# Optimization experiments

Measured on AMD Instinct MI355X. Metric: run time of the kernel, lower is better.

Reference implementation:

```python
import jax, jax.numpy as jnp
import numpy as np

N_NODES = 50000
N_EDGES = 800000
IN_FEATS = 128
H_FEATS = 128
OUT_FEATS = 64


def _mean_agg(h, src, dst, n_nodes):
    # mean over in-neighbors: sum h[src] into dst, divide by in-degree (0 for isolated nodes)
    summed = jax.ops.segment_sum(h[src], dst, num_segments=n_nodes)  # [N, d]
    deg = jax.ops.segment_sum(jnp.ones((src.shape[0],), h.dtype), dst, num_segments=n_nodes)
    return summed / jnp.maximum(deg, 1.0)[:, None]


def setup_inputs() -> dict:
    key = jax.random.key(0)
    ks = jax.random.split(key, 10)
    s = 0.05
    return {
        "inputs": jax.random.normal(ks[0], (N_NODES, IN_FEATS), jnp.float32),
        "fc_W": jax.random.normal(ks[1], (H_FEATS, IN_FEATS), jnp.float32) * s,
        "fc_b": jax.random.normal(ks[2], (H_FEATS,), jnp.float32) * s,
        "W": jax.random.normal(ks[3], (3, H_FEATS, H_FEATS), jnp.float32) * s,
        "b": jax.random.normal(ks[4], (3, H_FEATS), jnp.float32) * s,
        "W_last": jax.random.normal(ks[5], (OUT_FEATS, H_FEATS), jnp.float32) * s,
        "b_last": jax.random.normal(ks[6], (OUT_FEATS,), jnp.float32) * s,
        "eps": jnp.zeros((4,), jnp.float32),
        "src": jax.random.randint(ks[7], (N_EDGES,), 0, N_NODES, jnp.int32),
        "dst": jax.random.randint(ks[8], (N_EDGES,), 0, N_NODES, jnp.int32),
    }


def reference(inputs, fc_W, fc_b, W, b, W_last, b_last, eps, src, dst):
    n = inputs.shape[0]
    # input SLP
    h = jax.nn.relu(inputs @ fc_W.T + fc_b)
    # 3 hidden GIN layers: relu(Linear((1+eps)*h + mean_agg(h)))  (dropout = eval identity)
    for i in range(3):
        agg = _mean_agg(h, src, dst, n)
        h = jax.nn.relu(((1.0 + eps[i]) * h + agg) @ W[i].T + b[i])
    # last GIN layer (no ReLU)
    agg = _mean_agg(h, src, dst, n)
    h = ((1.0 + eps[3]) * h + agg) @ W_last.T + b_last
    return h
```

## Files before the change

### kernel.cpp

```cpp
#include <hip/hip_runtime.h>

#define N_NODES 50000
#define N_EDGES 800000
#define NBUCK 196
#define CAP 4608
#define CSTRIDE 16
#define EPB 2048
#define NSTRIPE ((N_EDGES + EPB - 1) / EPB)

typedef __attribute__((ext_vector_type(8))) short short8;
typedef __attribute__((ext_vector_type(4))) float float4v;

__device__ inline unsigned short f2bf(float f) {
    unsigned u = __float_as_uint(f);
    unsigned r = u + 0x7fff + ((u >> 16) & 1);
    return (unsigned short)(r >> 16);
}
__device__ inline float bf2f(unsigned short h) {
    return __uint_as_float(((unsigned)h) << 16);
}


__global__ void __launch_bounds__(256) wsplit_init(
    const float* __restrict__ fcW, const float* __restrict__ W, const float* __restrict__ Wl,
    unsigned short* __restrict__ hi, unsigned short* __restrict__ lo) {
    int i = blockIdx.x * 256 + threadIdx.x;
    float v;
    if (i < 16384) v = fcW[i];
    else if (i < 65536) v = W[i - 16384];
    else if (i < 73728) v = Wl[i - 65536];
    else return;
    unsigned short h = f2bf(v);
    hi[i] = h;
    lo[i] = f2bf(v - bf2f(h));
}


template <int COLS, bool RELU, bool WRITE_BF, bool BIAS, bool ASPLIT>
__device__ __forceinline__ void gemm_body(int bx, const float* __restrict__ U,
                                          const unsigned short* __restrict__ Uhi,
                                          const unsigned short* __restrict__ Ulo,
                                          const unsigned short* __restrict__ Whi,
                                          const unsigned short* __restrict__ Wlo,
                                          const float* __restrict__ bias, float* __restrict__ out,
                                          unsigned short* __restrict__ outbf, int nrows) {
    int wave = threadIdx.x >> 6;
    int lane = threadIdx.x & 63;
    int m = lane & 15;
    int quad = lane >> 4;
    int r0 = bx * 64 + wave * 16;
    int rowA = r0 + m;
    if (rowA >= nrows) rowA = nrows - 1;

    short8 ahi[4], alo[4];
    if (ASPLIT) {
        const unsigned short* hp = Uhi + (size_t)rowA * 128 + quad * 8;
        const unsigned short* lp = Ulo + (size_t)rowA * 128 + quad * 8;
#pragma unroll
        for (int kc = 0; kc < 4; kc++) {
            ahi[kc] = *(const short8*)(hp + kc * 32);
            alo[kc] = *(const short8*)(lp + kc * 32);
        }
    } else {
        const float* arow = U + (size_t)rowA * 128 + quad * 8;
#pragma unroll
        for (int kc = 0; kc < 4; kc++) {
            float4 f0 = *(const float4*)(arow + kc * 32);
            float4 f1 = *(const float4*)(arow + kc * 32 + 4);
            float fv[8] = {f0.x, f0.y, f0.z, f0.w, f1.x, f1.y, f1.z, f1.w};
#pragma unroll
            for (int j = 0; j < 8; j++) {
                unsigned short h = f2bf(fv[j]);
                ahi[kc][j] = (short)h;
                alo[kc][j] = (short)f2bf(fv[j] - bf2f(h));
            }
        }
    }

#pragma unroll
    for (int nt = 0; nt < COLS / 16; nt++) {
        int n = nt * 16 + m;
        const unsigned short* bhp = Whi + (size_t)n * 128 + quad * 8;
        const unsigned short* blp = Wlo + (size_t)n * 128 + quad * 8;
        float4v acc = {0.f, 0.f, 0.f, 0.f};
#pragma unroll
        for (int kc = 0; kc < 4; kc++) {
            short8 bh = *(const short8*)(bhp + kc * 32);
            short8 bl = *(const short8*)(blp + kc * 32);
            acc = __builtin_amdgcn_mfma_f32_16x16x32_bf16(ahi[kc], bh, acc, 0, 0, 0);
            acc = __builtin_amdgcn_mfma_f32_16x16x32_bf16(alo[kc], bh, acc, 0, 0, 0);
            acc = __builtin_amdgcn_mfma_f32_16x16x32_bf16(ahi[kc], bl, acc, 0, 0, 0);
        }
        float bv = 0.f;
        if (BIAS) bv = bias[n];
#pragma unroll
        for (int i = 0; i < 4; i++) {
            int r = r0 + quad * 4 + i;
            if (r < nrows) {
                float v = acc[i] + bv;
                if (RELU) v = fmaxf(v, 0.f);
                out[(size_t)r * COLS + n] = v;
                if (WRITE_BF) outbf[(size_t)r * COLS + n] = f2bf(v);
            }
        }
    }
}

template <int COLS, bool RELU, bool WRITE_BF, bool BIAS, bool ASPLIT>
__global__ void __launch_bounds__(256) gemm_mfma(const float* __restrict__ U,
                                                 const unsigned short* __restrict__ Uhi,
                                                 const unsigned short* __restrict__ Ulo,
                                                 const unsigned short* __restrict__ Whi,
                                                 const unsigned short* __restrict__ Wlo,
                                                 const float* __restrict__ bias,
                                                 float* __restrict__ out,
                                                 unsigned short* __restrict__ outbf, int nrows) {
    gemm_body<COLS, RELU, WRITE_BF, BIAS, ASPLIT>(blockIdx.x, U, Uhi, Ulo, Whi, Wlo, bias, out,
                                                  outbf, nrows);
}


__global__ void __launch_bounds__(256) fused_binA_gemm(
    const int* __restrict__ src, const int* __restrict__ dst, int* __restrict__ cursor,
    int* __restrict__ packed, const float* __restrict__ X, const unsigned short* __restrict__ whi,
    const unsigned short* __restrict__ wlo, const float* __restrict__ fcb, float* __restrict__ h,
    unsigned short* __restrict__ hbf) {
    int bx = blockIdx.x;
    if (bx < NSTRIPE) {
        __shared__ int lcount[256];
        __shared__ int lbase[256];
        int t = threadIdx.x;
        lcount[t] = 0;
        __syncthreads();
        int base = bx * EPB + t;
        int d[EPB / 256];
#pragma unroll
        for (int k = 0; k < EPB / 256; k++) {
            int i = base + k * 256;
            d[k] = (i < N_EDGES) ? dst[i] : -1;
            if (d[k] >= 0) atomicAdd(&lcount[((unsigned)d[k]) >> 8], 1);
        }
        __syncthreads();
        if (t < NBUCK) {
            lbase[t] = t * CAP + atomicAdd(&cursor[t * CSTRIDE], lcount[t]);
            lcount[t] = 0;
        }
        __syncthreads();
#pragma unroll
        for (int k = 0; k < EPB / 256; k++) {
            if (d[k] >= 0) {
                int i = base + k * 256;
                int wb = ((unsigned)d[k]) >> 8;
                int p = lbase[wb] + atomicAdd(&lcount[wb], 1);
                if (p < (wb + 1) * CAP)
                    packed[p] = ((d[k] & 255) << 16) | src[i];
            }
        }
    } else {
        gemm_body<128, true, true, true, false>(bx - NSTRIPE, X, nullptr, nullptr, whi, wlo, fcb,
                                                h, hbf, N_NODES);
    }
}


__global__ void __launch_bounds__(256) binB_kernel(const int* __restrict__ packed,
                                                   const int* __restrict__ cursor,
                                                   int* __restrict__ row_ptr,
                                                   int* __restrict__ esrc) {
    __shared__ int sm[256];
    __shared__ int cntS[256];
    __shared__ int curs[256];
    int b = blockIdx.x;
    int t = threadIdx.x;
    int cnt = (t < NBUCK) ? cursor[t * CSTRIDE] : 0;
    cntS[t] = cnt;
    sm[t] = cnt;
    __syncthreads();
    for (int o = 1; o < 256; o <<= 1) {
        int x = sm[t];
        int a = (t >= o) ? sm[t - o] : 0;
        __syncthreads();
        sm[t] = x + a;
        __syncthreads();
    }
    int w0 = sm[b] - cntS[b];
    int mycnt = cntS[b];
    int total = sm[NBUCK - 1];
    __syncthreads();
    if (b == NBUCK - 1 && t == 0) row_ptr[N_NODES] = total;
    int e0r = b * CAP, e1r = b * CAP + mycnt;
    curs[t] = 0;
    __syncthreads();
    for (int i = e0r + t; i < e1r; i += 256) atomicAdd(&curs[((unsigned)packed[i]) >> 16], 1);
    __syncthreads();
    int v = curs[t];
    sm[t] = v;
    __syncthreads();
    for (int o = 1; o < 256; o <<= 1) {
        int x = sm[t];
        int a = (t >= o) ? sm[t - o] : 0;
        __syncthreads();
        sm[t] = x + a;
        __syncthreads();
    }
    int excl = sm[t] - v;
    curs[t] = excl;
    int node = b * 256 + t;
    if (node < N_NODES) row_ptr[node] = w0 + excl;
    __syncthreads();
    for (int i = e0r + t; i < e1r; i += 256) {
        unsigned w = (unsigned)packed[i];
        int p = atomicAdd(&curs[w >> 16], 1);
        esrc[w0 + p] = (int)(w & 0xFFFFu);
    }
}


__global__ void __launch_bounds__(256) agg_kernel(
    const float* __restrict__ h, const unsigned short* __restrict__ hbf,
    const int* __restrict__ row_ptr, const int* __restrict__ esrc,
    const float* __restrict__ eps, int layer, unsigned* __restrict__ uhi32,
    unsigned* __restrict__ ulo32) {
    int gtid = blockIdx.x * 256 + threadIdx.x;
    int node = gtid >> 6;
    int lane = threadIdx.x & 63;
    if (node >= N_NODES) return;
    node = __builtin_amdgcn_readfirstlane(node);
    int beg = __builtin_amdgcn_readfirstlane(row_ptr[node]);
    int end = __builtin_amdgcn_readfirstlane(row_ptr[node + 1]);
    int eg = lane >> 4;
    int fo = lane & 15;

    float acc[8] = {0.f, 0.f, 0.f, 0.f, 0.f, 0.f, 0.f, 0.f};
    float acc2[8] = {0.f, 0.f, 0.f, 0.f, 0.f, 0.f, 0.f, 0.f};
    int e = beg;
    for (; e + 7 < end; e += 8) {
        int s0 = esrc[e + eg];
        int s1 = esrc[e + 4 + eg];
        short8 v0 = *(const short8*)(hbf + (size_t)s0 * 128 + fo * 8);
        short8 v1 = *(const short8*)(hbf + (size_t)s1 * 128 + fo * 8);
#pragma unroll
        for (int j = 0; j < 8; j++) acc[j] += bf2f((unsigned short)v0[j]);
#pragma unroll
        for (int j = 0; j < 8; j++) acc2[j] += bf2f((unsigned short)v1[j]);
    }
    if (e + 3 < end) {
        int s = esrc[e + eg];
        short8 v = *(const short8*)(hbf + (size_t)s * 128 + fo * 8);
#pragma unroll
        for (int j = 0; j < 8; j++) acc[j] += bf2f((unsigned short)v[j]);
        e += 4;
    }
    int rem = end - e;
    if (eg < rem) {
        int s = esrc[e + eg];
        short8 v = *(const short8*)(hbf + (size_t)s * 128 + fo * 8);
#pragma unroll
        for (int j = 0; j < 8; j++) acc2[j] += bf2f((unsigned short)v[j]);
    }
#pragma unroll
    for (int j = 0; j < 8; j++) {
        acc[j] += acc2[j];
        acc[j] += __shfl_xor(acc[j], 16);
        acc[j] += __shfl_xor(acc[j], 32);
    }
    if (eg == 0) {
        int d = end - beg;
        float inv = (d > 0) ? 1.0f / (float)d : 0.0f;
        float ep = 1.0f + eps[layer];
        const float* hr = h + (size_t)node * 128 + fo * 8;
        float4 h0 = *(const float4*)hr;
        float4 h1 = *(const float4*)(hr + 4);
        float hv[8] = {h0.x, h0.y, h0.z, h0.w, h1.x, h1.y, h1.z, h1.w};
        unsigned hip[4], lop[4];
#pragma unroll
        for (int jj = 0; jj < 4; jj++) {
            float ux = ep * hv[2 * jj] + acc[2 * jj] * inv;
            float uy = ep * hv[2 * jj + 1] + acc[2 * jj + 1] * inv;
            unsigned short uh0 = f2bf(ux), uh1 = f2bf(uy);
            hip[jj] = (unsigned)uh0 | ((unsigned)uh1 << 16);
            lop[jj] = (unsigned)f2bf(ux - bf2f(uh0)) | ((unsigned)f2bf(uy - bf2f(uh1)) << 16);
        }
        uint4* ph = (uint4*)(uhi32 + (size_t)node * 64 + fo * 4);
        uint4* pl = (uint4*)(ulo32 + (size_t)node * 64 + fo * 4);
        *ph = make_uint4(hip[0], hip[1], hip[2], hip[3]);
        *pl = make_uint4(lop[0], lop[1], lop[2], lop[3]);
    }
}


__global__ void __launch_bounds__(256) agg64_out(
    const float* __restrict__ g, const unsigned short* __restrict__ gbf,
    const int* __restrict__ row_ptr, const int* __restrict__ esrc,
    const float* __restrict__ eps, const float* __restrict__ bl, float* __restrict__ out) {
    int gtid = blockIdx.x * 256 + threadIdx.x;
    int node = gtid >> 6;
    if (node >= N_NODES) return;
    int lane = threadIdx.x & 63;
    node = __builtin_amdgcn_readfirstlane(node);
    int beg = __builtin_amdgcn_readfirstlane(row_ptr[node]);
    int end = __builtin_amdgcn_readfirstlane(row_ptr[node + 1]);
    int eg = lane >> 3;
    int fo = lane & 7;

    float acc[8] = {0.f, 0.f, 0.f, 0.f, 0.f, 0.f, 0.f, 0.f};
    float acc2[8] = {0.f, 0.f, 0.f, 0.f, 0.f, 0.f, 0.f, 0.f};
    int e = beg;
    for (; e + 15 < end; e += 16) {
        int s0 = esrc[e + eg];
        int s1 = esrc[e + 8 + eg];
        short8 v0 = *(const short8*)(gbf + (size_t)s0 * 64 + fo * 8);
        short8 v1 = *(const short8*)(gbf + (size_t)s1 * 64 + fo * 8);
#pragma unroll
        for (int j = 0; j < 8; j++) acc[j] += bf2f((unsigned short)v0[j]);
#pragma unroll
        for (int j = 0; j < 8; j++) acc2[j] += bf2f((unsigned short)v1[j]);
    }
    if (e + 7 < end) {
        int s = esrc[e + eg];
        short8 v = *(const short8*)(gbf + (size_t)s * 64 + fo * 8);
#pragma unroll
        for (int j = 0; j < 8; j++) acc[j] += bf2f((unsigned short)v[j]);
        e += 8;
    }
    int rem = end - e;
    if (eg < rem) {
        int s = esrc[e + eg];
        short8 v = *(const short8*)(gbf + (size_t)s * 64 + fo * 8);
#pragma unroll
        for (int j = 0; j < 8; j++) acc2[j] += bf2f((unsigned short)v[j]);
    }
#pragma unroll
    for (int j = 0; j < 8; j++) {
        acc[j] += acc2[j];
        acc[j] += __shfl_xor(acc[j], 8);
        acc[j] += __shfl_xor(acc[j], 16);
        acc[j] += __shfl_xor(acc[j], 32);
    }
    if (eg == 0) {
        int d = end - beg;
        float inv = (d > 0) ? 1.0f / (float)d : 0.0f;
        float ep = 1.0f + eps[3];
        const float* gr = g + (size_t)node * 64 + fo * 8;
        float4 g0 = *(const float4*)gr;
        float4 g1 = *(const float4*)(gr + 4);
        const float* blr = bl + fo * 8;
        float4 b0 = *(const float4*)blr;
        float4 b1 = *(const float4*)(blr + 4);
        float4 r0, r1;
        r0.x = ep * g0.x + acc[0] * inv + b0.x;
        r0.y = ep * g0.y + acc[1] * inv + b0.y;
        r0.z = ep * g0.z + acc[2] * inv + b0.z;
        r0.w = ep * g0.w + acc[3] * inv + b0.w;
        r1.x = ep * g1.x + acc[4] * inv + b1.x;
        r1.y = ep * g1.y + acc[5] * inv + b1.y;
        r1.z = ep * g1.z + acc[6] * inv + b1.z;
        r1.w = ep * g1.w + acc[7] * inv + b1.w;
        float* op = out + (size_t)node * 64 + fo * 8;
        *(float4*)op = r0;
        *(float4*)(op + 4) = r1;
    }
}


extern "C" void kernel_launch(void* const* d_in, const int* in_sizes, int n_in,
                              void* d_out, int out_size, void* d_ws, size_t ws_size,
                              hipStream_t stream) {
    const float* X   = (const float*)d_in[0];
    const float* fcW = (const float*)d_in[1];
    const float* fcb = (const float*)d_in[2];
    const float* W   = (const float*)d_in[3];
    const float* b   = (const float*)d_in[4];
    const float* Wl  = (const float*)d_in[5];
    const float* bl  = (const float*)d_in[6];
    const float* eps = (const float*)d_in[7];
    const int* src   = (const int*)d_in[8];
    const int* dst   = (const int*)d_in[9];
    float* out = (float*)d_out;

    float* h = (float*)d_ws;
    unsigned short* hbf = (unsigned short*)(h + (size_t)N_NODES * 128);
    unsigned short* uhi = hbf + (size_t)N_NODES * 128;
    unsigned short* ulo = uhi + (size_t)N_NODES * 128;
    unsigned short* whi = ulo + (size_t)N_NODES * 128;
    unsigned short* wlo = whi + 73728;
    int* cursor  = (int*)(wlo + 73728);
    int* row_ptr = cursor + NBUCK * CSTRIDE;
    int* packed  = row_ptr + N_NODES + 1;
    int* esrc    = packed + NBUCK * CAP;
    float* g = (float*)uhi;
    unsigned short* gbf = ulo;

    const int gemm_blocks = (N_NODES + 63) / 64;
    const int agg_blocks = (N_NODES * 64 + 255) / 256;
    const int prep_blocks = (73728 + 255) / 256;

    hipMemsetAsync(cursor, 0, NBUCK * CSTRIDE * sizeof(int), stream);
    wsplit_init<<<prep_blocks, 256, 0, stream>>>(fcW, W, Wl, whi, wlo);
    fused_binA_gemm<<<NSTRIPE + gemm_blocks, 256, 0, stream>>>(src, dst, cursor, packed, X, whi,
                                                               wlo, fcb, h, hbf);
    binB_kernel<<<NBUCK, 256, 0, stream>>>(packed, cursor, row_ptr, esrc);

    for (int i = 0; i < 3; i++) {
        agg_kernel<<<agg_blocks, 256, 0, stream>>>(h, hbf, row_ptr, esrc, eps, i,
                                                   (unsigned*)uhi, (unsigned*)ulo);
        if (i < 2)
            gemm_mfma<128, true, true, true, true><<<gemm_blocks, 256, 0, stream>>>(
                nullptr, uhi, ulo, whi + 16384 + (size_t)i * 16384,
                wlo + 16384 + (size_t)i * 16384, b + (size_t)i * 128, h, hbf, N_NODES);
        else
            gemm_mfma<128, true, false, true, true><<<gemm_blocks, 256, 0, stream>>>(
                nullptr, uhi, ulo, whi + 16384 + (size_t)i * 16384,
                wlo + 16384 + (size_t)i * 16384, b + (size_t)i * 128, h, nullptr, N_NODES);
    }

    gemm_mfma<64, false, true, false, false><<<gemm_blocks, 256, 0, stream>>>(
        h, nullptr, nullptr, whi + 65536, wlo + 65536, nullptr, g, gbf, N_NODES);
    agg64_out<<<agg_blocks, 256, 0, stream>>>(g, gbf, row_ptr, esrc, eps, bl, out);
}
```

Before: 410.3 us.

## Fuse last hidden GEMM with output projection and deepen aggregation unrolling

Layer 3's 128x128 GEMM and the final 128->64 projection now run in one kernel. The ReLU'd hidden tile is split into bf16 hi/lo and staged in swizzled LDS, so h no longer makes a round trip through global memory and one launch is removed. The aggregation kernels use four independent accumulator sets with 16/32-edge unrolled gathers to keep more loads in flight. The cursor memset is folded into the weight-split kernel, and the binning stripe size is doubled without holding dst values in registers. Risks are higher register and LDS pressure, and g/gbf reusing the uhi/hbf buffers relies on each block reading its rows before writing them.

```diff
diff --git a/kernel.cpp b/kernel.cpp
--- a/kernel.cpp
+++ b/kernel.cpp
@@ -5,7 +5,7 @@
 #define NBUCK 196
 #define CAP 4608
 #define CSTRIDE 16
-#define EPB 2048
+#define EPB 4096
 #define NSTRIPE ((N_EDGES + EPB - 1) / EPB)
 
 typedef __attribute__((ext_vector_type(8))) short short8;
@@ -23,7 +23,10 @@
 
 __global__ void __launch_bounds__(256) wsplit_init(
     const float* __restrict__ fcW, const float* __restrict__ W, const float* __restrict__ Wl,
-    unsigned short* __restrict__ hi, unsigned short* __restrict__ lo) {
+    unsigned short* __restrict__ hi, unsigned short* __restrict__ lo, int* __restrict__ cursor) {
+    if (blockIdx.x == 0) {
+        for (int j = threadIdx.x; j < NBUCK * CSTRIDE; j += 256) cursor[j] = 0;
+    }
     int i = blockIdx.x * 256 + threadIdx.x;
     float v;
     if (i < 16384) v = fcW[i];
@@ -120,6 +123,98 @@
 }
 
 
+__global__ void __launch_bounds__(256) gemm_last_fused(
+    const unsigned short* __restrict__ Uhi, const unsigned short* __restrict__ Ulo,
+    const unsigned short* __restrict__ Whi, const unsigned short* __restrict__ Wlo,
+    const float* __restrict__ bias, const unsigned short* __restrict__ Lhi,
+    const unsigned short* __restrict__ Llo, float* __restrict__ g,
+    unsigned short* __restrict__ gbf) {
+    __shared__ unsigned short lds_hi[64 * 128];
+    __shared__ unsigned short lds_lo[64 * 128];
+    int bx = blockIdx.x;
+    int wave = threadIdx.x >> 6;
+    int lane = threadIdx.x & 63;
+    int m = lane & 15;
+    int quad = lane >> 4;
+    int r0 = bx * 64 + wave * 16;
+    int rowA = r0 + m;
+    if (rowA >= N_NODES) rowA = N_NODES - 1;
+
+    short8 ahi[4], alo[4];
+    {
+        const unsigned short* hp = Uhi + (size_t)rowA * 128 + quad * 8;
+        const unsigned short* lp = Ulo + (size_t)rowA * 128 + quad * 8;
+#pragma unroll
+        for (int kc = 0; kc < 4; kc++) {
+            ahi[kc] = *(const short8*)(hp + kc * 32);
+            alo[kc] = *(const short8*)(lp + kc * 32);
+        }
+    }
+#pragma unroll
+    for (int nt = 0; nt < 8; nt++) {
+        int n = nt * 16 + m;
+        const unsigned short* bhp = Whi + (size_t)n * 128 + quad * 8;
+        const unsigned short* blp = Wlo + (size_t)n * 128 + quad * 8;
+        float4v acc = {0.f, 0.f, 0.f, 0.f};
+#pragma unroll
+        for (int kc = 0; kc < 4; kc++) {
+            short8 bh = *(const short8*)(bhp + kc * 32);
+            short8 bl = *(const short8*)(blp + kc * 32);
+            acc = __builtin_amdgcn_mfma_f32_16x16x32_bf16(ahi[kc], bh, acc, 0, 0, 0);
+            acc = __builtin_amdgcn_mfma_f32_16x16x32_bf16(alo[kc], bh, acc, 0, 0, 0);
+            acc = __builtin_amdgcn_mfma_f32_16x16x32_bf16(ahi[kc], bl, acc, 0, 0, 0);
+        }
+        float bv = bias[n];
+#pragma unroll
+        for (int i = 0; i < 4; i++) {
+            int rl = wave * 16 + quad * 4 + i;
+            float v = fmaxf(acc[i] + bv, 0.f);
+            unsigned short vh = f2bf(v);
+            unsigned short vl = f2bf(v - bf2f(vh));
+            int idx = rl * 128 + (n ^ ((rl & 7) << 3));
+            lds_hi[idx] = vh;
+            lds_lo[idx] = vl;
+        }
+    }
+    __syncthreads();
+
+    short8 ahi2[4], alo2[4];
+    {
+        int rl = wave * 16 + m;
+#pragma unroll
+        for (int kc = 0; kc < 4; kc++) {
+            int idx = rl * 128 + ((kc * 32 + quad * 8) ^ ((rl & 7) << 3));
+            ahi2[kc] = *(const short8*)&lds_hi[idx];
+            alo2[kc] = *(const short8*)&lds_lo[idx];
+        }
+    }
+#pragma unroll
+    for (int nt = 0; nt < 4; nt++) {
+        int n = nt * 16 + m;
+        const unsigned short* bhp = Lhi + (size_t)n * 128 + quad * 8;
+        const unsigned short* blp = Llo + (size_t)n * 128 + quad * 8;
+        float4v acc = {0.f, 0.f, 0.f, 0.f};
+#pragma unroll
+        for (int kc = 0; kc < 4; kc++) {
+            short8 bh = *(const short8*)(bhp + kc * 32);
+            short8 bl = *(const short8*)(blp + kc * 32);
+            acc = __builtin_amdgcn_mfma_f32_16x16x32_bf16(ahi2[kc], bh, acc, 0, 0, 0);
+            acc = __builtin_amdgcn_mfma_f32_16x16x32_bf16(alo2[kc], bh, acc, 0, 0, 0);
+            acc = __builtin_amdgcn_mfma_f32_16x16x32_bf16(ahi2[kc], bl, acc, 0, 0, 0);
+        }
+#pragma unroll
+        for (int i = 0; i < 4; i++) {
+            int r = r0 + quad * 4 + i;
+            if (r < N_NODES) {
+                float v = acc[i];
+                g[(size_t)r * 64 + n] = v;
+                gbf[(size_t)r * 64 + n] = f2bf(v);
+            }
+        }
+    }
+}
+
+
 __global__ void __launch_bounds__(256) fused_binA_gemm(
     const int* __restrict__ src, const int* __restrict__ dst, int* __restrict__ cursor,
     int* __restrict__ packed, const float* __restrict__ X, const unsigned short* __restrict__ whi,
@@ -133,12 +228,10 @@
         lcount[t] = 0;
         __syncthreads();
         int base = bx * EPB + t;
-        int d[EPB / 256];
-#pragma unroll
+#pragma unroll 4
         for (int k = 0; k < EPB / 256; k++) {
             int i = base + k * 256;
-            d[k] = (i < N_EDGES) ? dst[i] : -1;
-            if (d[k] >= 0) atomicAdd(&lcount[((unsigned)d[k]) >> 8], 1);
+            if (i < N_EDGES) atomicAdd(&lcount[((unsigned)dst[i]) >> 8], 1);
         }
         __syncthreads();
         if (t < NBUCK) {
@@ -146,14 +239,15 @@
             lcount[t] = 0;
         }
         __syncthreads();
-#pragma unroll
+#pragma unroll 4
         for (int k = 0; k < EPB / 256; k++) {
-            if (d[k] >= 0) {
-                int i = base + k * 256;
-                int wb = ((unsigned)d[k]) >> 8;
+            int i = base + k * 256;
+            if (i < N_EDGES) {
+                int d = dst[i];
+                int wb = ((unsigned)d) >> 8;
                 int p = lbase[wb] + atomicAdd(&lcount[wb], 1);
                 if (p < (wb + 1) * CAP)
-                    packed[p] = ((d[k] & 255) << 16) | src[i];
+                    packed[p] = ((d & 255) << 16) | src[i];
             }
         }
     } else {
@@ -231,24 +325,45 @@
     int eg = lane >> 4;
     int fo = lane & 15;
 
-    float acc[8] = {0.f, 0.f, 0.f, 0.f, 0.f, 0.f, 0.f, 0.f};
-    float acc2[8] = {0.f, 0.f, 0.f, 0.f, 0.f, 0.f, 0.f, 0.f};
+    float a0[8] = {0.f, 0.f, 0.f, 0.f, 0.f, 0.f, 0.f, 0.f};
+    float a1[8] = {0.f, 0.f, 0.f, 0.f, 0.f, 0.f, 0.f, 0.f};
+    float a2[8] = {0.f, 0.f, 0.f, 0.f, 0.f, 0.f, 0.f, 0.f};
+    float a3[8] = {0.f, 0.f, 0.f, 0.f, 0.f, 0.f, 0.f, 0.f};
     int e = beg;
-    for (; e + 7 < end; e += 8) {
+    for (; e + 15 < end; e += 16) {
+        int s0 = esrc[e + eg];
+        int s1 = esrc[e + 4 + eg];
+        int s2 = esrc[e + 8 + eg];
+        int s3 = esrc[e + 12 + eg];
+        short8 v0 = *(const short8*)(hbf + (size_t)s0 * 128 + fo * 8);
+        short8 v1 = *(const short8*)(hbf + (size_t)s1 * 128 + fo * 8);
+        short8 v2 = *(const short8*)(hbf + (size_t)s2 * 128 + fo * 8);
+        short8 v3 = *(const short8*)(hbf + (size_t)s3 * 128 + fo * 8);
+#pragma unroll
+        for (int j = 0; j < 8; j++) a0[j] += bf2f((unsigned short)v0[j]);
+#pragma unroll
+        for (int j = 0; j < 8; j++) a1[j] += bf2f((unsigned short)v1[j]);
+#pragma unroll
+        for (int j = 0; j < 8; j++) a2[j] += bf2f((unsigned short)v2[j]);
+#pragma unroll
+        for (int j = 0; j < 8; j++) a3[j] += bf2f((unsigned short)v3[j]);
+    }
+    if (e + 7 < end) {
         int s0 = esrc[e + eg];
         int s1 = esrc[e + 4 + eg];
         short8 v0 = *(const short8*)(hbf + (size_t)s0 * 128 + fo * 8);
         short8 v1 = *(const short8*)(hbf + (size_t)s1 * 128 + fo * 8);
 #pragma unroll
-        for (int j = 0; j < 8; j++) acc[j] += bf2f((unsigned short)v0[j]);
-#pragma unroll
-        for (int j = 0; j < 8; j++) acc2[j] += bf2f((unsigned short)v1[j]);
+        for (int j = 0; j < 8; j++) a0[j] += bf2f((unsigned short)v0[j]);
+#pragma unroll
+        for (int j = 0; j < 8; j++) a1[j] += bf2f((unsigned short)v1[j]);
+        e += 8;
     }
     if (e + 3 < end) {
         int s = esrc[e + eg];
         short8 v = *(const short8*)(hbf + (size_t)s * 128 + fo * 8);
 #pragma unroll
-        for (int j = 0; j < 8; j++) acc[j] += bf2f((unsigned short)v[j]);
+        for (int j = 0; j < 8; j++) a2[j] += bf2f((unsigned short)v[j]);
         e += 4;
     }
     int rem = end - e;
@@ -256,13 +371,14 @@
         int s = esrc[e + eg];
         short8 v = *(const short8*)(hbf + (size_t)s * 128 + fo * 8);
 #pragma unroll
-        for (int j = 0; j < 8; j++) acc2[j] += bf2f((unsigned short)v[j]);
+        for (int j = 0; j < 8; j++) a3[j] += bf2f((unsigned short)v[j]);
     }
 #pragma unroll
     for (int j = 0; j < 8; j++) {
-        acc[j] += acc2[j];
-        acc[j] += __shfl_xor(acc[j], 16);
-        acc[j] += __shfl_xor(acc[j], 32);
+        float s = (a0[j] + a1[j]) + (a2[j] + a3[j]);
+        s += __shfl_xor(s, 16);
+        s += __shfl_xor(s, 32);
+        a0[j] = s;
     }
     if (eg == 0) {
         int d = end - beg;
@@ -275,8 +391,8 @@
         unsigned hip[4], lop[4];
 #pragma unroll
         for (int jj = 0; jj < 4; jj++) {
-            float ux = ep * hv[2 * jj] + acc[2 * jj] * inv;
-            float uy = ep * hv[2 * jj + 1] + acc[2 * jj + 1] * inv;
+            float ux = ep * hv[2 * jj] + a0[2 * jj] * inv;
+            float uy = ep * hv[2 * jj + 1] + a0[2 * jj + 1] * inv;
             unsigned short uh0 = f2bf(ux), uh1 = f2bf(uy);
             hip[jj] = (unsigned)uh0 | ((unsigned)uh1 << 16);
             lop[jj] = (unsigned)f2bf(ux - bf2f(uh0)) | ((unsigned)f2bf(uy - bf2f(uh1)) << 16);
@@ -303,24 +419,45 @@
     int eg = lane >> 3;
     int fo = lane & 7;
 
-    float acc[8] = {0.f, 0.f, 0.f, 0.f, 0.f, 0.f, 0.f, 0.f};
-    float acc2[8] = {0.f, 0.f, 0.f, 0.f, 0.f, 0.f, 0.f, 0.f};
+    float a0[8] = {0.f, 0.f, 0.f, 0.f, 0.f, 0.f, 0.f, 0.f};
+    float a1[8] = {0.f, 0.f, 0.f, 0.f, 0.f, 0.f, 0.f, 0.f};
+    float a2[8] = {0.f, 0.f, 0.f, 0.f, 0.f, 0.f, 0.f, 0.f};
+    float a3[8] = {0.f, 0.f, 0.f, 0.f, 0.f, 0.f, 0.f, 0.f};
     int e = beg;
-    for (; e + 15 < end; e += 16) {
+    for (; e + 31 < end; e += 32) {
+        int s0 = esrc[e + eg];
+        int s1 = esrc[e + 8 + eg];
+        int s2 = esrc[e + 16 + eg];
+        int s3 = esrc[e + 24 + eg];
+        short8 v0 = *(const short8*)(gbf + (size_t)s0 * 64 + fo * 8);
+        short8 v1 = *(const short8*)(gbf + (size_t)s1 * 64 + fo * 8);
+        short8 v2 = *(const short8*)(gbf + (size_t)s2 * 64 + fo * 8);
+        short8 v3 = *(const short8*)(gbf + (size_t)s3 * 64 + fo * 8);
+#pragma unroll
+        for (int j = 0; j < 8; j++) a0[j] += bf2f((unsigned short)v0[j]);
+#pragma unroll
+        for (int j = 0; j < 8; j++) a1[j] += bf2f((unsigned short)v1[j]);
+#pragma unroll
+        for (int j = 0; j < 8; j++) a2[j] += bf2f((unsigned short)v2[j]);
+#pragma unroll
+        for (int j = 0; j < 8; j++) a3[j] += bf2f((unsigned short)v3[j]);
+    }
+    if (e + 15 < end) {
         int s0 = esrc[e + eg];
         int s1 = esrc[e + 8 + eg];
         short8 v0 = *(const short8*)(gbf + (size_t)s0 * 64 + fo * 8);
         short8 v1 = *(const short8*)(gbf + (size_t)s1 * 64 + fo * 8);
 #pragma unroll
-        for (int j = 0; j < 8; j++) acc[j] += bf2f((unsigned short)v0[j]);
-#pragma unroll
-        for (int j = 0; j < 8; j++) acc2[j] += bf2f((unsigned short)v1[j]);
+        for (int j = 0; j < 8; j++) a0[j] += bf2f((unsigned short)v0[j]);
+#pragma unroll
+        for (int j = 0; j < 8; j++) a1[j] += bf2f((unsigned short)v1[j]);
+        e += 16;
     }
     if (e + 7 < end) {
         int s = esrc[e + eg];
         short8 v = *(const short8*)(gbf + (size_t)s * 64 + fo * 8);
 #pragma unroll
-        for (int j = 0; j < 8; j++) acc[j] += bf2f((unsigned short)v[j]);
+        for (int j = 0; j < 8; j++) a2[j] += bf2f((unsigned short)v[j]);
         e += 8;
     }
     int rem = end - e;
@@ -328,14 +465,15 @@
         int s = esrc[e + eg];
         short8 v = *(const short8*)(gbf + (size_t)s * 64 + fo * 8);
 #pragma unroll
-        for (int j = 0; j < 8; j++) acc2[j] += bf2f((unsigned short)v[j]);
+        for (int j = 0; j < 8; j++) a3[j] += bf2f((unsigned short)v[j]);
     }
 #pragma unroll
     for (int j = 0; j < 8; j++) {
-        acc[j] += acc2[j];
-        acc[j] += __shfl_xor(acc[j], 8);
-        acc[j] += __shfl_xor(acc[j], 16);
-        acc[j] += __shfl_xor(acc[j], 32);
+        float s = (a0[j] + a1[j]) + (a2[j] + a3[j]);
+        s += __shfl_xor(s, 8);
+        s += __shfl_xor(s, 16);
+        s += __shfl_xor(s, 32);
+        a0[j] = s;
     }
     if (eg == 0) {
         int d = end - beg;
@@ -348,14 +486,14 @@
         float4 b0 = *(const float4*)blr;
         float4 b1 = *(const float4*)(blr + 4);
         float4 r0, r1;
-        r0.x = ep * g0.x + acc[0] * inv + b0.x;
-        r0.y = ep * g0.y + acc[1] * inv + b0.y;
-        r0.z = ep * g0.z + acc[2] * inv + b0.z;
-        r0.w = ep * g0.w + acc[3] * inv + b0.w;
-        r1.x = ep * g1.x + acc[4] * inv + b1.x;
-        r1.y = ep * g1.y + acc[5] * inv + b1.y;
-        r1.z = ep * g1.z + acc[6] * inv + b1.z;
-        r1.w = ep * g1.w + acc[7] * inv + b1.w;
+        r0.x = ep * g0.x + a0[0] * inv + b0.x;
+        r0.y = ep * g0.y + a0[1] * inv + b0.y;
+        r0.z = ep * g0.z + a0[2] * inv + b0.z;
+        r0.w = ep * g0.w + a0[3] * inv + b0.w;
+        r1.x = ep * g1.x + a0[4] * inv + b1.x;
+        r1.y = ep * g1.y + a0[5] * inv + b1.y;
+        r1.z = ep * g1.z + a0[6] * inv + b1.z;
+        r1.w = ep * g1.w + a0[7] * inv + b1.w;
         float* op = out + (size_t)node * 64 + fo * 8;
         *(float4*)op = r0;
         *(float4*)(op + 4) = r1;
@@ -389,32 +527,29 @@
     int* packed  = row_ptr + N_NODES + 1;
     int* esrc    = packed + NBUCK * CAP;
     float* g = (float*)uhi;
-    unsigned short* gbf = ulo;
+    unsigned short* gbf = hbf;
 
     const int gemm_blocks = (N_NODES + 63) / 64;
     const int agg_blocks = (N_NODES * 64 + 255) / 256;
     const int prep_blocks = (73728 + 255) / 256;
 
-    hipMemsetAsync(cursor, 0, NBUCK * CSTRIDE * sizeof(int), stream);
-    wsplit_init<<<prep_blocks, 256, 0, stream>>>(fcW, W, Wl, whi, wlo);
+    wsplit_init<<<prep_blocks, 256, 0, stream>>>(fcW, W, Wl, whi, wlo, cursor);
     fused_binA_gemm<<<NSTRIPE + gemm_blocks, 256, 0, stream>>>(src, dst, cursor, packed, X, whi,
                                                                wlo, fcb, h, hbf);
     binB_kernel<<<NBUCK, 256, 0, stream>>>(packed, cursor, row_ptr, esrc);
 
-    for (int i = 0; i < 3; i++) {
+    for (int i = 0; i < 2; i++) {
         agg_kernel<<<agg_blocks, 256, 0, stream>>>(h, hbf, row_ptr, esrc, eps, i,
                                                    (unsigned*)uhi, (unsigned*)ulo);
-        if (i < 2)
-            gemm_mfma<128, true, true, true, true><<<gemm_blocks, 256, 0, stream>>>(
-                nullptr, uhi, ulo, whi + 16384 + (size_t)i * 16384,
-                wlo + 16384 + (size_t)i * 16384, b + (size_t)i * 128, h, hbf, N_NODES);
-        else
-            gemm_mfma<128, true, false, true, true><<<gemm_blocks, 256, 0, stream>>>(
-                nullptr, uhi, ulo, whi + 16384 + (size_t)i * 16384,
-                wlo + 16384 + (size_t)i * 16384, b + (size_t)i * 128, h, nullptr, N_NODES);
-    }
-
-    gemm_mfma<64, false, true, false, false><<<gemm_blocks, 256, 0, stream>>>(
-        h, nullptr, nullptr, whi + 65536, wlo + 65536, nullptr, g, gbf, N_NODES);
+        gemm_mfma<128, true, true, true, true><<<gemm_blocks, 256, 0, stream>>>(
+            nullptr, uhi, ulo, whi + 16384 + (size_t)i * 16384,
+            wlo + 16384 + (size_t)i * 16384, b + (size_t)i * 128, h, hbf, N_NODES);
+    }
+
+    agg_kernel<<<agg_blocks, 256, 0, stream>>>(h, hbf, row_ptr, esrc, eps, 2,
+                                               (unsigned*)uhi, (unsigned*)ulo);
+    gemm_last_fused<<<gemm_blocks, 256, 0, stream>>>(uhi, ulo, whi + 49152, wlo + 49152,
+                                                     b + 256, whi + 65536, wlo + 65536, g, gbf);
+
     agg64_out<<<agg_blocks, 256, 0, stream>>>(g, gbf, row_ptr, esrc, eps, bl, out);
 }
```

New measurement: 395.8 us. 1.04x faster.
